# Performance work log

Hardware: AMD Instinct MI355X
Metric: run time of the kernel (lower is better)

Reference implementation:

```python
import jax, jax.numpy as jnp
import numpy as np

E = 1024
H = 16
HD = E // H
FF = 4 * E
B, T = 2, 2048


def _linear_params(key, fan_in, fan_out):
    k1, k2 = jax.random.split(key)
    bound = 1.0 / np.sqrt(fan_in)
    W = jax.random.uniform(k1, (fan_out, fan_in), jnp.float32, -bound, bound)
    b = jax.random.uniform(k2, (fan_out,), jnp.float32, -bound, bound)
    return W, b


def setup_inputs() -> dict:
    key = jax.random.key(0)
    keys = jax.random.split(key, 8)
    x = jax.random.normal(keys[0], (B, T, E), jnp.float32)
    Wq, bq = _linear_params(keys[1], E, E)
    Wk, bk = _linear_params(keys[2], E, E)
    Wv, bv = _linear_params(keys[3], E, E)
    Wo, bo = _linear_params(keys[4], E, E)
    W1, b1 = _linear_params(keys[5], E, FF)
    W2, b2 = _linear_params(keys[6], FF, E)
    ln1_g = jnp.ones((E,), jnp.float32); ln1_b = jnp.zeros((E,), jnp.float32)
    ln2_g = jnp.ones((E,), jnp.float32); ln2_b = jnp.zeros((E,), jnp.float32)
    return {"x": x, "Wq": Wq, "bq": bq, "Wk": Wk, "bk": bk, "Wv": Wv, "bv": bv,
            "Wo": Wo, "bo": bo, "W1": W1, "b1": b1, "W2": W2, "b2": b2,
            "ln1_g": ln1_g, "ln1_b": ln1_b, "ln2_g": ln2_g, "ln2_b": ln2_b}


def _layernorm(x, g, b, eps=1e-5):
    mu = jnp.mean(x, axis=-1, keepdims=True)
    var = jnp.var(x, axis=-1, keepdims=True)
    return (x - mu) * jax.lax.rsqrt(var + eps) * g + b


def reference(x, Wq, bq, Wk, bk, Wv, bv, Wo, bo, W1, b1, W2, b2,
              ln1_g, ln1_b, ln2_g, ln2_b):
    Bc, Tc, Ec = x.shape
    h = _layernorm(x, ln1_g, ln1_b)
    # projections (torch Linear: y = x @ W.T + b)
    q = (h @ Wq.T + bq).reshape(Bc, Tc, H, HD).transpose(0, 2, 1, 3)  # [B,H,T,hd]
    k = (h @ Wk.T + bk).reshape(Bc, Tc, H, HD).transpose(0, 2, 1, 3)
    v = (h @ Wv.T + bv).reshape(Bc, Tc, H, HD).transpose(0, 2, 1, 3)
    scores = jnp.einsum('bhqd,bhkd->bhqk', q, k) / np.sqrt(HD).astype(np.float32)
    causal = jnp.tril(jnp.ones((Tc, Tc), bool))
    scores = jnp.where(causal, scores, -jnp.inf)
    att = jax.nn.softmax(scores, axis=-1)  # dropout = identity (eval)
    out = jnp.einsum('bhqk,bhkd->bhqd', att, v)
    out = out.transpose(0, 2, 1, 3).reshape(Bc, Tc, Ec)
    x = x + out @ Wo.T + bo
    h2 = _layernorm(x, ln2_g, ln2_b)
    ff = jax.nn.relu(h2 @ W1.T + b1) @ W2.T + b2
    return x + ff
```

## Files before the change

### kernel.cpp

```cpp
#include <hip/hip_runtime.h>

typedef unsigned short u16;
typedef __bf16 bf16x8 __attribute__((ext_vector_type(8)));
typedef float f32x4 __attribute__((ext_vector_type(4)));

#define E_ 1024
#define T_ 2048
#define B_ 2
#define H_ 16
#define FF_ 4096
#define M_ 4096

__device__ __forceinline__ u16 f2b(float f) {
    union { float f; unsigned u; } c; c.f = f;
    unsigned r = c.u + 0x7FFFu + ((c.u >> 16) & 1u);
    return (u16)(r >> 16);
}
__device__ __forceinline__ u16 f2bt(float f) {
    union { float f; unsigned u; } c; c.f = f;
    return (u16)(c.u >> 16);
}

__device__ __forceinline__ void gl16(const u16* g, u16* l) {
    __builtin_amdgcn_global_load_lds(
        (__attribute__((address_space(1))) void*)g,
        (__attribute__((address_space(3))) void*)l, 16, 0, 0);
}

template<int N> __device__ __forceinline__ void wait_vmcnt() {
    if constexpr (N == 2)      asm volatile("s_waitcnt vmcnt(2)" ::: "memory");
    else if constexpr (N == 3) asm volatile("s_waitcnt vmcnt(3)" ::: "memory");
    else if constexpr (N == 4) asm volatile("s_waitcnt vmcnt(4)" ::: "memory");
    else                       asm volatile("s_waitcnt vmcnt(0)" ::: "memory");
}

__global__ __launch_bounds__(256) void cvt_ln(
        const float* __restrict__ Wq, const float* __restrict__ Wk,
        const float* __restrict__ Wv, const float* __restrict__ Wo,
        const float* __restrict__ W1, const float* __restrict__ W2,
        const float* __restrict__ bq, const float* __restrict__ bk,
        const float* __restrict__ bv,
        u16* __restrict__ WqkvB, u16* __restrict__ WoB,
        u16* __restrict__ W1B, u16* __restrict__ W2B,
        float* __restrict__ bqkv,
        const float* __restrict__ x, const float* __restrict__ g1,
        const float* __restrict__ b1v, u16* __restrict__ hB) {
    if (blockIdx.x < 1024) {
        int row = blockIdx.x * 4 + (threadIdx.x >> 6);
        int t = threadIdx.x & 63;
        const float* xr = x + (size_t)row * E_;
        float v[16];
        float sum = 0.f, ss = 0.f;
#pragma unroll
        for (int c = 0; c < 4; c++) {
            float4 f = *(const float4*)&xr[c * 256 + t * 4];
            v[c * 4 + 0] = f.x; v[c * 4 + 1] = f.y; v[c * 4 + 2] = f.z; v[c * 4 + 3] = f.w;
            sum += f.x + f.y + f.z + f.w;
            ss += f.x * f.x + f.y * f.y + f.z * f.z + f.w * f.w;
        }
#pragma unroll
        for (int d = 32; d; d >>= 1) {
            sum += __shfl_xor(sum, d);
            ss  += __shfl_xor(ss, d);
        }
        float mu = sum * (1.f / E_);
        float var = ss * (1.f / E_) - mu * mu;
        float rs = rsqrtf(var + 1e-5f);
#pragma unroll
        for (int c = 0; c < 4; c++) {
            int idx = c * 256 + t * 4;
            float4 g4 = *(const float4*)&g1[idx];
            float4 b4 = *(const float4*)&b1v[idx];
            ushort4 o;
            o.x = f2b((v[c * 4 + 0] - mu) * rs * g4.x + b4.x);
            o.y = f2b((v[c * 4 + 1] - mu) * rs * g4.y + b4.y);
            o.z = f2b((v[c * 4 + 2] - mu) * rs * g4.z + b4.z);
            o.w = f2b((v[c * 4 + 3] - mu) * rs * g4.w + b4.w);
            *(ushort4*)&hB[(size_t)row * E_ + idx] = o;
        }
        return;
    }
    int i = (blockIdx.x - 1024) * 256 + threadIdx.x;
    if (i >= 3146496) return;
    if (i >= 3145728) {
        int j = i - 3145728;
        const float* s = (j < 256) ? bq : (j < 512) ? bk : bv;
        int jj = j & 255;
        *(float4*)&bqkv[j * 4] = *(const float4*)&s[jj * 4];
        return;
    }
    const float* src; u16* dst; int j;
    if (i < 786432) {
        src = (i < 262144) ? Wq : (i < 524288) ? Wk : Wv;
        j = i & 262143;
        dst = WqkvB + (i >> 18) * (E_ * E_);
    } else if (i < 1048576) { j = i - 786432;  src = Wo; dst = WoB; }
    else if (i < 2097152)   { j = i - 1048576; src = W1; dst = W1B; }
    else                    { j = i - 2097152; src = W2; dst = W2B; }
    float4 f = *(const float4*)&src[j * 4];
    ushort4 o;
    o.x = f2b(f.x); o.y = f2b(f.y); o.z = f2b(f.z); o.w = f2b(f.w);
    *(ushort4*)&dst[j * 4] = o;
}

__global__ __launch_bounds__(64) void ln_fwd(u16* __restrict__ out, const float* __restrict__ x,
                                             const float* __restrict__ g, const float* __restrict__ bta) {
    int row = blockIdx.x;
    int t = threadIdx.x;
    const float* xr = x + (size_t)row * E_;
    float v[16];
    float sum = 0.f, ss = 0.f;
#pragma unroll
    for (int c = 0; c < 4; c++) {
        float4 f = *(const float4*)&xr[c * 256 + t * 4];
        v[c * 4 + 0] = f.x; v[c * 4 + 1] = f.y; v[c * 4 + 2] = f.z; v[c * 4 + 3] = f.w;
        sum += f.x + f.y + f.z + f.w;
        ss += f.x * f.x + f.y * f.y + f.z * f.z + f.w * f.w;
    }
#pragma unroll
    for (int d = 32; d; d >>= 1) {
        sum += __shfl_xor(sum, d);
        ss  += __shfl_xor(ss, d);
    }
    float mu = sum * (1.f / E_);
    float var = ss * (1.f / E_) - mu * mu;
    float rs = rsqrtf(var + 1e-5f);
#pragma unroll
    for (int c = 0; c < 4; c++) {
        int idx = c * 256 + t * 4;
        float4 g4 = *(const float4*)&g[idx];
        float4 b4 = *(const float4*)&bta[idx];
        ushort4 o;
        o.x = f2b((v[c * 4 + 0] - mu) * rs * g4.x + b4.x);
        o.y = f2b((v[c * 4 + 1] - mu) * rs * g4.y + b4.y);
        o.z = f2b((v[c * 4 + 2] - mu) * rs * g4.z + b4.z);
        o.w = f2b((v[c * 4 + 3] - mu) * rs * g4.w + b4.w);
        *(ushort4*)&out[(size_t)row * E_ + idx] = o;
    }
}

template<int QKV, int SPLIT>
__global__ __launch_bounds__(512, 2) void gemm256(
        const u16* __restrict__ A, const u16* __restrict__ Bt,
        const float* __restrict__ bias, const float* __restrict__ residual,
        float* __restrict__ outF, float* __restrict__ oP1,
        float* __restrict__ oP2, float* __restrict__ oP3,
        u16* __restrict__ outB, u16* __restrict__ outVt,
        int N, int K, int ldk, int relu) {
    __shared__ __align__(16) u16 As[2][256 * 64];
    __shared__ __align__(16) u16 Bs[2][256 * 64];
    int tid = threadIdx.x;
    int bx = blockIdx.x, by = blockIdx.y;
    {
        int gx = gridDim.x;
        int nwg = gx * (int)gridDim.y, cpx = nwg >> 3;
        int lin = by * gx + bx;
        int wv = (lin & 7) * cpx + (lin >> 3);
        bx = wv % gx; by = wv / gx;
    }
    int m0 = by * 256, n0 = bx * 256;
    int kz = blockIdx.z;
    int koff = kz * K;
    int w = tid >> 6, lane = tid & 63;
    int wm = w >> 2, wn = w & 3;
    int r16 = lane & 15, kg = lane >> 4;
    int sw = (r16 & 7) << 3;

    int srow = tid >> 3;
    int schunk = (tid & 7) ^ (srow & 7);
    const u16* gAs = A + (size_t)(m0 + srow) * ldk + koff + schunk * 8;
    const u16* gBs = Bt + (size_t)(n0 + srow) * ldk + koff + schunk * 8;
    size_t rstep = (size_t)64 * ldk;

    f32x4 acc[8][4] = {};
    const int nk = K >> 6;

    auto stA = [&](int kt, int b, int r0, int r1) {
        const u16* g = gAs + kt * 64;
        u16* l = &As[b][0] + tid * 8;
        gl16(g + (size_t)r0 * rstep, l + r0 * 4096);
        gl16(g + (size_t)r1 * rstep, l + r1 * 4096);
    };
    auto stB = [&](int kt, int b, int r0, int r1) {
        const u16* g = gBs + kt * 64;
        u16* l = &Bs[b][0] + tid * 8;
        gl16(g + (size_t)r0 * rstep, l + r0 * 4096);
        gl16(g + (size_t)r1 * rstep, l + r1 * 4096);
    };

    stB(0, 0, 0, 1); stB(0, 0, 2, 3); stA(0, 0, 0, 2); stA(0, 0, 1, 3);
    asm volatile("s_waitcnt vmcnt(0)" ::: "memory");
    __builtin_amdgcn_s_barrier();
    asm volatile("" ::: "memory");

    for (int t = 0; t < nk; t++) {
        int cb = t & 1, nb = cb ^ 1;
        const bool pf = (t + 1 < nk);
        bf16x8 bfr[4];
#pragma unroll
        for (int ph = 0; ph < 4; ph++) {
            const int kk = ph >> 1, mh = ph & 1;
            int ce = kk * 32 + kg * 8;
            if (mh == 0) {
#pragma unroll
                for (int nf = 0; nf < 4; nf++) {
                    int row = wn * 64 + nf * 16 + r16;
                    bfr[nf] = *(const bf16x8*)&Bs[cb][(row * 64 + ce) ^ sw];
                }
            }
            bf16x8 af[4];
#pragma unroll
            for (int i = 0; i < 4; i++) {
                int row = wm * 128 + (mh * 4 + i) * 16 + r16;
                af[i] = *(const bf16x8*)&As[cb][(row * 64 + ce) ^ sw];
            }
            if (pf) {
                if (ph == 0)      { stB(t + 1, nb, 0, 1); stB(t + 1, nb, 2, 3); }
                else if (ph == 1) { stA(t + 1, nb, 0, 2); stA(t + 1, nb, 1, 3); }
            }
            __builtin_amdgcn_s_barrier();
            asm volatile("s_waitcnt lgkmcnt(0)" ::: "memory");
            __builtin_amdgcn_s_setprio(1);
#pragma unroll
            for (int i = 0; i < 4; i++)
#pragma unroll
                for (int nf = 0; nf < 4; nf++)
                    acc[mh * 4 + i][nf] = __builtin_amdgcn_mfma_f32_16x16x32_bf16(
                        af[i], bfr[nf], acc[mh * 4 + i][nf], 0, 0, 0);
            __builtin_amdgcn_s_setprio(0);
            if (ph == 3 && pf)
                asm volatile("s_waitcnt vmcnt(0)" ::: "memory");
            __builtin_amdgcn_s_barrier();
            asm volatile("" ::: "memory");
        }
    }

#pragma unroll
    for (int mf = 0; mf < 8; mf++) {
#pragma unroll
        for (int nf = 0; nf < 4; nf++) {
            int gm = m0 + wm * 128 + mf * 16 + kg * 4;
            int gn = n0 + wn * 64 + nf * 16 + r16;
            float bv = bias[gn];
            if (QKV) {
                if (gn < 2048) {
                    float scl = (gn < 1024) ? 0.18033688f : 1.0f;
#pragma unroll
                    for (int r = 0; r < 4; r++)
                        outB[(size_t)(gm + r) * 2048 + gn] = f2b((acc[mf][nf][r] + bv) * scl);
                } else {
                    int bq_ = gm >> 11, tq = gm & 2047, d = gn - 2048;
                    ushort4 ov;
                    ov.x = f2b(acc[mf][nf][0] + bv);
                    ov.y = f2b(acc[mf][nf][1] + bv);
                    ov.z = f2b(acc[mf][nf][2] + bv);
                    ov.w = f2b(acc[mf][nf][3] + bv);
                    *(ushort4*)&outVt[((size_t)(bq_ * 1024 + d)) * 2048 + tq] = ov;
                }
            } else if (SPLIT) {
                float* po = (kz == 1) ? oP1 : (kz == 2) ? oP2 : oP3;
#pragma unroll
                for (int r = 0; r < 4; r++) {
                    size_t off = (size_t)(gm + r) * N + gn;
                    if (kz == 0) {
                        float v = acc[mf][nf][r] + bv;
                        if (residual) v += residual[off];
                        outF[off] = v;
                    } else {
                        po[off] = acc[mf][nf][r];
                    }
                }
            } else {
#pragma unroll
                for (int r = 0; r < 4; r++) {
                    float v = acc[mf][nf][r] + bv;
                    if (relu) v = fmaxf(v, 0.f);
                    outB[(size_t)(gm + r) * N + gn] = f2b(v);
                }
            }
        }
    }
}

template<int BM, int BN>
__global__ __launch_bounds__(256) void gemm_bt(
        const u16* __restrict__ A, const u16* __restrict__ Bt,
        const float* __restrict__ bias, const float* __restrict__ residual,
        float* __restrict__ outF, float* __restrict__ oP1,
        float* __restrict__ oP2, float* __restrict__ oP3,
        u16* __restrict__ outB, u16* __restrict__ outVt,
        int M, int N, int K, int ldk, int relu, int qkvmode, int swz) {
    constexpr int MT = BM / 32, NT = BN / 32;
    constexpr int LA = BM / 64, LB = BN / 64;
    __shared__ __align__(16) u16 As[3][BM * 32];
    __shared__ __align__(16) u16 Bs[3][BN * 32];
    int tid = threadIdx.x;
    int bx = blockIdx.x, by = blockIdx.y;
    if (swz) {
        int gx = gridDim.x;
        int nwg = gx * gridDim.y;
        int lin = by * gx + bx;
        int wv = (lin & 7) * (nwg >> 3) + (lin >> 3);
        bx = wv % gx; by = wv / gx;
    }
    int m0 = by * BM, n0 = bx * BN;
    int kz = blockIdx.z;
    int koff = kz * K;
    int wave = tid >> 6, lane = tid & 63;
    int wm = wave & 1, wn = wave >> 1;
    int r16 = lane & 15, kg = lane >> 4;

    const u16* gA = A + (size_t)(m0 + wave * (BM / 4) + (lane >> 2)) * ldk + koff + (lane & 3) * 8;
    const u16* gB = Bt + (size_t)(n0 + wave * (BN / 4) + (lane >> 2)) * ldk + koff + (lane & 3) * 8;
    size_t row16 = (size_t)16 * ldk;
    int aoff = wave * (BM / 4) * 32;
    int boff = wave * (BN / 4) * 32;

    f32x4 acc[MT][NT] = {};

    const int nk = K >> 5;

    auto issue = [&](int kt, int buf) {
        int k1 = kt << 5;
        gl16(gA + k1, As[buf] + aoff);
        if (LA == 2) gl16(gA + k1 + row16, As[buf] + aoff + 512);
        gl16(gB + k1, Bs[buf] + boff);
        if (LB == 2) gl16(gB + k1 + row16, Bs[buf] + boff + 512);
    };

    auto compute = [&](int cb) {
        bf16x8 af[MT], bfr[NT];
#pragma unroll
        for (int mt = 0; mt < MT; mt++)
            af[mt] = *(const bf16x8*)&As[cb][(wm * (BM / 2) + mt * 16 + r16) * 32 + kg * 8];
#pragma unroll
        for (int nt = 0; nt < NT; nt++)
            bfr[nt] = *(const bf16x8*)&Bs[cb][(wn * (BN / 2) + nt * 16 + r16) * 32 + kg * 8];
#pragma unroll
        for (int mt = 0; mt < MT; mt++)
#pragma unroll
            for (int nt = 0; nt < NT; nt++)
                acc[mt][nt] = __builtin_amdgcn_mfma_f32_16x16x32_bf16(af[mt], bfr[nt], acc[mt][nt], 0, 0, 0);
    };

    issue(0, 0);
    issue(1, 1);

    int cur = 0;
    for (int ks = 0; ks < nk - 1; ks++) {
        wait_vmcnt<LA + LB>();
        __builtin_amdgcn_s_barrier();
        asm volatile("" ::: "memory");
        if (ks + 2 < nk) {
            int p2 = cur ? cur - 1 : 2;
            issue(ks + 2, p2);
        }
        compute(cur);
        cur = (cur < 2) ? cur + 1 : 0;
    }
    asm volatile("s_waitcnt vmcnt(0)" ::: "memory");
    __builtin_amdgcn_s_barrier();
    asm volatile("" ::: "memory");
    compute(cur);

#pragma unroll
    for (int mt = 0; mt < MT; mt++) {
#pragma unroll
        for (int nt = 0; nt < NT; nt++) {
            int gm = m0 + wm * (BM / 2) + mt * 16 + kg * 4;
            int gn = n0 + wn * (BN / 2) + nt * 16 + r16;
            float bv = bias[gn];
            if (qkvmode) {
                if (gn < 2048) {
                    float scl = (gn < 1024) ? 0.18033688f : 1.0f;
#pragma unroll
                    for (int r = 0; r < 4; r++)
                        outB[(size_t)(gm + r) * 2048 + gn] = f2b((acc[mt][nt][r] + bv) * scl);
                } else {
                    int bq_ = gm >> 11, tq = gm & 2047, d = gn - 2048;
                    ushort4 ov;
                    ov.x = f2b(acc[mt][nt][0] + bv);
                    ov.y = f2b(acc[mt][nt][1] + bv);
                    ov.z = f2b(acc[mt][nt][2] + bv);
                    ov.w = f2b(acc[mt][nt][3] + bv);
                    *(ushort4*)&outVt[((size_t)(bq_ * 1024 + d)) * 2048 + tq] = ov;
                }
            } else if (oP1) {
                float* po = (kz == 1) ? oP1 : (kz == 2) ? oP2 : oP3;
#pragma unroll
                for (int r = 0; r < 4; r++) {
                    size_t off = (size_t)(gm + r) * N + gn;
                    if (kz == 0) {
                        float v = acc[mt][nt][r] + bv;
                        if (residual) v += residual[off];
                        outF[off] = v;
                    } else {
                        po[off] = acc[mt][nt][r];
                    }
                }
            } else {
#pragma unroll
                for (int r = 0; r < 4; r++) {
                    float v = acc[mt][nt][r] + bv;
                    size_t off = (size_t)(gm + r) * N + gn;
                    if (residual) v += residual[off];
                    if (relu) v = fmaxf(v, 0.f);
                    if (outF) outF[off] = v;
                    else outB[off] = f2b(v);
                }
            }
        }
    }
}

__global__ __launch_bounds__(256) void addf3(float* __restrict__ d, const float* __restrict__ a,
                                             const float* __restrict__ b, const float* __restrict__ c) {
    size_t i = ((size_t)blockIdx.x * 256 + threadIdx.x) * 4;
    float4 vd = *(float4*)&d[i];
    float4 va = *(const float4*)&a[i];
    float4 vb = *(const float4*)&b[i];
    float4 vc = *(const float4*)&c[i];
    vd.x += va.x + vb.x + vc.x;
    vd.y += va.y + vb.y + vc.y;
    vd.z += va.z + vb.z + vc.z;
    vd.w += va.w + vb.w + vc.w;
    *(float4*)&d[i] = vd;
}

#define AST 68
__global__ __launch_bounds__(256) void attn_mfma(
        const u16* __restrict__ qk, const u16* __restrict__ vt,
        u16* __restrict__ out) {
    __shared__ __align__(16) u16 Ks[2][64 * AST];
    __shared__ __align__(16) u16 Vs[2][64 * AST];
    __shared__ __align__(16) u16 Ps[4][16 * AST];

    int bz = blockIdx.x;
    int h  = bz & 15;
    int b  = (bz >> 4) & 1;
    int qt = bz >> 5;

    int tid = threadIdx.x;
    int w = tid >> 6, lane = tid & 63;
    int g = lane >> 4, l16 = lane & 15;

    int qrow = qt * 64 + w * 16 + l16;
    bf16x8 qf[2];
    qf[0] = *(const bf16x8*)&qk[(size_t)(b * T_ + qrow) * 2048 + h * 64 + g * 8];
    qf[1] = *(const bf16x8*)&qk[(size_t)(b * T_ + qrow) * 2048 + h * 64 + 32 + g * 8];

    f32x4 o[4] = {};
    f32x4 lp = {0.f, 0.f, 0.f, 0.f};

    int r1 = tid >> 3, col1 = (tid & 7) * 8;
    const u16* gK = qk + (size_t)(b * T_) * 2048 + 1024 + h * 64;
    const u16* gV = vt + (size_t)(b * 1024 + h * 64) * 2048;

    uint4 kr1 = *(const uint4*)&gK[(size_t)r1 * 2048 + col1];
    uint4 kr2 = *(const uint4*)&gK[(size_t)(r1 + 32) * 2048 + col1];
    uint4 vr1 = *(const uint4*)&gV[(size_t)r1 * 2048 + col1];
    uint4 vr2 = *(const uint4*)&gV[(size_t)(r1 + 32) * 2048 + col1];

    for (int t = 0; t <= qt; t++) {
        int cur = t & 1;
        *(uint4*)&Ks[cur][r1 * AST + col1] = kr1;
        *(uint4*)&Ks[cur][(r1 + 32) * AST + col1] = kr2;
        *(uint4*)&Vs[cur][r1 * AST + col1] = vr1;
        *(uint4*)&Vs[cur][(r1 + 32) * AST + col1] = vr2;
        __syncthreads();
        if (t < qt) {
            int j1 = (t + 1) * 64;
            kr1 = *(const uint4*)&gK[(size_t)(j1 + r1) * 2048 + col1];
            kr2 = *(const uint4*)&gK[(size_t)(j1 + r1 + 32) * 2048 + col1];
            vr1 = *(const uint4*)&gV[(size_t)r1 * 2048 + j1 + col1];
            vr2 = *(const uint4*)&gV[(size_t)(r1 + 32) * 2048 + j1 + col1];
        }

        f32x4 s[4];
#pragma unroll
        for (int nt = 0; nt < 4; nt++) {
            f32x4 c16 = {-16.f, -16.f, -16.f, -16.f};
            bf16x8 k0 = *(const bf16x8*)&Ks[cur][(nt * 16 + l16) * AST + g * 8];
            bf16x8 k1 = *(const bf16x8*)&Ks[cur][(nt * 16 + l16) * AST + 32 + g * 8];
            s[nt] = __builtin_amdgcn_mfma_f32_16x16x32_bf16(qf[0], k0, c16, 0, 0, 0);
            s[nt] = __builtin_amdgcn_mfma_f32_16x16x32_bf16(qf[1], k1, s[nt], 0, 0, 0);
        }

        if (t == qt) {
            int j0 = t * 64;
#pragma unroll
            for (int nt = 0; nt < 4; nt++) {
                int key = j0 + nt * 16 + l16;
#pragma unroll
                for (int r = 0; r < 4; r++) {
                    int q = qt * 64 + w * 16 + g * 4 + r;
                    if (key > q) s[nt][r] = -INFINITY;
                }
            }
        }

#pragma unroll
        for (int nt = 0; nt < 4; nt++)
#pragma unroll
            for (int r = 0; r < 4; r++) {
                float p = exp2f(s[nt][r]);
                lp[r] += p;
                Ps[w][(g * 4 + r) * AST + nt * 16 + l16] = f2bt(p);
            }

#pragma unroll
        for (int kf = 0; kf < 2; kf++) {
            bf16x8 pf = *(const bf16x8*)&Ps[w][l16 * AST + kf * 32 + g * 8];
#pragma unroll
            for (int nt = 0; nt < 4; nt++) {
                bf16x8 vf = *(const bf16x8*)&Vs[cur][(nt * 16 + l16) * AST + kf * 32 + g * 8];
                o[nt] = __builtin_amdgcn_mfma_f32_16x16x32_bf16(pf, vf, o[nt], 0, 0, 0);
            }
        }
    }

#pragma unroll
    for (int x = 1; x <= 8; x <<= 1)
#pragma unroll
        for (int r = 0; r < 4; r++)
            lp[r] += __shfl_xor(lp[r], x);

    float inv[4];
#pragma unroll
    for (int r = 0; r < 4; r++) inv[r] = 1.f / lp[r];
    int qg = qt * 64 + w * 16 + g * 4;
#pragma unroll
    for (int nt = 0; nt < 4; nt++)
#pragma unroll
        for (int r = 0; r < 4; r++)
            out[(size_t)(b * T_ + qg + r) * E_ + h * 64 + nt * 16 + l16] =
                f2b(o[nt][r] * inv[r]);
}

extern "C" void kernel_launch(void* const* d_in, const int* in_sizes, int n_in,
                              void* d_out, int out_size, void* d_ws, size_t ws_size,
                              hipStream_t stream) {
    const float* x    = (const float*)d_in[0];
    const float* Wq   = (const float*)d_in[1];
    const float* bq   = (const float*)d_in[2];
    const float* Wk   = (const float*)d_in[3];
    const float* bk   = (const float*)d_in[4];
    const float* Wv   = (const float*)d_in[5];
    const float* bv   = (const float*)d_in[6];
    const float* Wo   = (const float*)d_in[7];
    const float* bo   = (const float*)d_in[8];
    const float* W1   = (const float*)d_in[9];
    const float* b1   = (const float*)d_in[10];
    const float* W2   = (const float*)d_in[11];
    const float* b2   = (const float*)d_in[12];
    const float* ln1g = (const float*)d_in[13];
    const float* ln1b = (const float*)d_in[14];
    const float* ln2g = (const float*)d_in[15];
    const float* ln2b = (const float*)d_in[16];

    char* ws = (char*)d_ws;
    size_t off = 0;
    auto alloc = [&](size_t bytes) { char* p = ws + off; off += (bytes + 255) & ~(size_t)255; return p; };

    u16*   hB    = (u16*)  alloc((size_t)M_ * E_ * 2);
    u16*   WqkvB = (u16*)  alloc((size_t)3 * E_ * E_ * 2);
    u16*   WoB   = (u16*)  alloc((size_t)E_ * E_ * 2);
    u16*   W1B   = (u16*)  alloc((size_t)FF_ * E_ * 2);
    u16*   W2B   = (u16*)  alloc((size_t)E_ * FF_ * 2);
    float* bqkv  = (float*)alloc(3 * E_ * 4);
    u16*   qkB   = (u16*)  alloc((size_t)M_ * 2 * E_ * 2);
    u16*   vtG   = (u16*)  alloc((size_t)M_ * E_ * 2);
    u16*   attnB = (u16*)  alloc((size_t)M_ * E_ * 2);
    float* x2    = (float*)alloc((size_t)M_ * E_ * 4);
    u16*   h2B   = (u16*)  alloc((size_t)M_ * E_ * 2);
    u16*   rB    = (u16*)  alloc((size_t)M_ * FF_ * 2);
    float* P1    = (float*)alloc((size_t)M_ * E_ * 4);
    float* P2 = (float*)qkB;
    float* P3 = (float*)ws;

    cvt_ln<<<1024 + 12291, 256, 0, stream>>>(Wq, Wk, Wv, Wo, W1, W2, bq, bk, bv,
                                             WqkvB, WoB, W1B, W2B, bqkv,
                                             x, ln1g, ln1b, hB);

    gemm256<1, 0><<<dim3(3 * E_ / 256, M_ / 256), 512, 0, stream>>>(
        hB, WqkvB, bqkv, nullptr, nullptr, nullptr, nullptr, nullptr,
        qkB, vtG, 3 * E_, E_, E_, 0);

    attn_mfma<<<B_ * H_ * (T_ / 64), 256, 0, stream>>>(qkB, vtG, attnB);

    gemm_bt<64, 128><<<dim3(E_ / 128, M_ / 64), 256, 0, stream>>>(
        attnB, WoB, bo, x, x2, nullptr, nullptr, nullptr, nullptr, nullptr,
        M_, E_, E_, E_, 0, 0, 0);

    ln_fwd<<<M_, 64, 0, stream>>>(h2B, x2, ln2g, ln2b);

    gemm256<0, 0><<<dim3(FF_ / 256, M_ / 256), 512, 0, stream>>>(
        h2B, W1B, b1, nullptr, nullptr, nullptr, nullptr, nullptr,
        rB, nullptr, FF_, E_, E_, 1);

    gemm256<0, 1><<<dim3(E_ / 256, M_ / 256, 4), 512, 0, stream>>>(
        rB, W2B, b2, x2, (float*)d_out, P1, P2, P3,
        nullptr, nullptr, E_, FF_ / 4, FF_, 0);

    addf3<<<(M_ * E_) / (256 * 4), 256, 0, stream>>>((float*)d_out, P1, P2, P3);
}
```

Before: 398.4 us.

## Triple-buffer A tiles in GEMM and prefetch two k-steps ahead

The A operand's LDS staging grows from two to three buffers. A tiles are now prefetched two k-iterations ahead and B tiles one ahead, using vmcnt-based waits so the newest loads can stay in flight. The mid-phase barrier and explicit lgkmcnt wait are dropped, leaving one barrier per phase. This aims to hide global-load latency and cut synchronisation, at the cost of more LDS (160KB total) and more complex wait accounting.

New measurement: 428.2 us. 1.07x slower.

```diff
diff --git a/kernel.cpp b/kernel.cpp
--- a/kernel.cpp
+++ b/kernel.cpp
@@ -31,6 +31,7 @@
     if constexpr (N == 2)      asm volatile("s_waitcnt vmcnt(2)" ::: "memory");
     else if constexpr (N == 3) asm volatile("s_waitcnt vmcnt(3)" ::: "memory");
     else if constexpr (N == 4) asm volatile("s_waitcnt vmcnt(4)" ::: "memory");
+    else if constexpr (N == 8) asm volatile("s_waitcnt vmcnt(8)" ::: "memory");
     else                       asm volatile("s_waitcnt vmcnt(0)" ::: "memory");
 }
 
@@ -147,7 +148,7 @@
         float* __restrict__ oP2, float* __restrict__ oP3,
         u16* __restrict__ outB, u16* __restrict__ outVt,
         int N, int K, int ldk, int relu) {
-    __shared__ __align__(16) u16 As[2][256 * 64];
+    __shared__ __align__(16) u16 As[3][256 * 64];
     __shared__ __align__(16) u16 Bs[2][256 * 64];
     int tid = threadIdx.x;
     int bx = blockIdx.x, by = blockIdx.y;
@@ -175,51 +176,53 @@
     f32x4 acc[8][4] = {};
     const int nk = K >> 6;
 
-    auto stA = [&](int kt, int b, int r0, int r1) {
+    auto stA = [&](int kt, int slot, int r0, int r1) {
         const u16* g = gAs + kt * 64;
-        u16* l = &As[b][0] + tid * 8;
+        u16* l = &As[slot][0] + tid * 8;
         gl16(g + (size_t)r0 * rstep, l + r0 * 4096);
         gl16(g + (size_t)r1 * rstep, l + r1 * 4096);
     };
-    auto stB = [&](int kt, int b, int r0, int r1) {
+    auto stB = [&](int kt, int slot, int r0, int r1) {
         const u16* g = gBs + kt * 64;
-        u16* l = &Bs[b][0] + tid * 8;
+        u16* l = &Bs[slot][0] + tid * 8;
         gl16(g + (size_t)r0 * rstep, l + r0 * 4096);
         gl16(g + (size_t)r1 * rstep, l + r1 * 4096);
     };
 
     stB(0, 0, 0, 1); stB(0, 0, 2, 3); stA(0, 0, 0, 2); stA(0, 0, 1, 3);
-    asm volatile("s_waitcnt vmcnt(0)" ::: "memory");
+    stB(1, 1, 0, 1); stB(1, 1, 2, 3); stA(1, 1, 0, 2); stA(1, 1, 1, 3);
+    wait_vmcnt<8>();
     __builtin_amdgcn_s_barrier();
     asm volatile("" ::: "memory");
 
+    int ca = 0;
+    int sa2 = 2;
     for (int t = 0; t < nk; t++) {
-        int cb = t & 1, nb = cb ^ 1;
-        const bool pf = (t + 1 < nk);
+        int cbB = t & 1;
+        const bool pf1 = (t + 1 < nk), pf2 = (t + 2 < nk);
         bf16x8 bfr[4];
 #pragma unroll
         for (int ph = 0; ph < 4; ph++) {
             const int kk = ph >> 1, mh = ph & 1;
+            if (ph == 0 && t && pf1) {
+                stB(t + 1, cbB ^ 1, 0, 1); stB(t + 1, cbB ^ 1, 2, 3);
+            }
+            if (ph == 1 && pf2) stA(t + 2, sa2, 0, 2);
+            if (ph == 2 && pf2) stA(t + 2, sa2, 1, 3);
             int ce = kk * 32 + kg * 8;
             if (mh == 0) {
 #pragma unroll
                 for (int nf = 0; nf < 4; nf++) {
                     int row = wn * 64 + nf * 16 + r16;
-                    bfr[nf] = *(const bf16x8*)&Bs[cb][(row * 64 + ce) ^ sw];
+                    bfr[nf] = *(const bf16x8*)&Bs[cbB][(row * 64 + ce) ^ sw];
                 }
             }
             bf16x8 af[4];
 #pragma unroll
             for (int i = 0; i < 4; i++) {
                 int row = wm * 128 + (mh * 4 + i) * 16 + r16;
-                af[i] = *(const bf16x8*)&As[cb][(row * 64 + ce) ^ sw];
-            }
-            if (pf) {
-                if (ph == 0)      { stB(t + 1, nb, 0, 1); stB(t + 1, nb, 2, 3); }
-                else if (ph == 1) { stA(t + 1, nb, 0, 2); stA(t + 1, nb, 1, 3); }
-            }
-            __builtin_amdgcn_s_barrier();
-            asm volatile("s_waitcnt lgkmcnt(0)" ::: "memory");
+                af[i] = *(const bf16x8*)&As[ca][(row * 64 + ce) ^ sw];
+            }
             __builtin_amdgcn_s_setprio(1);
 #pragma unroll
             for (int i = 0; i < 4; i++)
@@ -228,11 +231,15 @@
                     acc[mh * 4 + i][nf] = __builtin_amdgcn_mfma_f32_16x16x32_bf16(
                         af[i], bfr[nf], acc[mh * 4 + i][nf], 0, 0, 0);
             __builtin_amdgcn_s_setprio(0);
-            if (ph == 3 && pf)
-                asm volatile("s_waitcnt vmcnt(0)" ::: "memory");
+            if (ph == 3) {
+                if (pf2) wait_vmcnt<4>();
+                else     wait_vmcnt<0>();
+            }
             __builtin_amdgcn_s_barrier();
             asm volatile("" ::: "memory");
         }
+        ca = (ca == 2) ? 0 : ca + 1;
+        sa2 = (sa2 == 2) ? 0 : sa2 + 1;
     }
 
 #pragma unroll
```
